# Kernel optimization log

Hardware: AMD Instinct MI355X
Metric: run time of the kernel (lower is better)

Reference implementation:

```python
import jax, jax.numpy as jnp
import numpy as np

N = 100_000   # nodes
E = 3_200_000 # edges
F = 13        # input features
H = 64        # hidden dim
G = 512       # graphs in batch
C = 2         # output classes
BN_EPS = 1e-5


def _linear(key, fan_in, fan_out):
    kw, kb = jax.random.split(key)
    bound = 1.0 / np.sqrt(fan_in)
    W = jax.random.uniform(kw, (fan_in, fan_out), jnp.float32, -bound, bound)
    b = jax.random.uniform(kb, (fan_out,), jnp.float32, -bound, bound)
    return W, b


def _conv_params(key, fin, fout):
    k1, k2, k3 = jax.random.split(key, 3)
    W1, b1 = _linear(k1, fin, fout)
    W2, b2 = _linear(k2, fout, fout)
    gamma = jnp.ones((fout,), jnp.float32)
    beta = jnp.zeros((fout,), jnp.float32)
    mean = jax.random.normal(k3, (fout,), jnp.float32) * 0.1
    var = jnp.ones((fout,), jnp.float32)
    return W1, b1, gamma, beta, mean, var, W2, b2


def setup_inputs() -> dict:
    key = jax.random.key(0)
    ks = jax.random.split(key, 10)
    x = jax.random.normal(ks[0], (N, F), jnp.float32)
    src = jax.random.randint(ks[1], (E,), 0, N, jnp.int32)
    dst = jax.random.randint(ks[2], (E,), 0, N, jnp.int32)
    batch = jnp.sort(jax.random.randint(ks[3], (N,), 0, G, jnp.int32))
    inp = {"x": x, "src": src, "dst": dst, "batch": batch}
    for i, name in enumerate(["c1", "c2", "c3"]):
        fin = F if i == 0 else H
        W1, b1, g, be, m, v, W2, b2 = _conv_params(ks[4 + i], fin, H)
        inp.update({f"{name}_W1": W1, f"{name}_b1": b1, f"{name}_g": g,
                    f"{name}_be": be, f"{name}_m": m, f"{name}_v": v,
                    f"{name}_W2": W2, f"{name}_b2": b2})
    inp["fc1_W"], inp["fc1_b"] = _linear(ks[7], 3 * H, 3 * H)
    inp["fc2_W"], inp["fc2_b"] = _linear(ks[8], 3 * H, C)
    return inp


def _mlp(h, W1, b1, g, be, m, v, W2, b2):
    # Linear -> BatchNorm1d (inference, running stats) -> ReLU -> Linear -> ReLU
    h = h @ W1 + b1
    h = (h - m) * jax.lax.rsqrt(v + BN_EPS) * g + be
    h = jax.nn.relu(h)
    return jax.nn.relu(h @ W2 + b2)


def _gin_conv(x, src, dst, mlp_params):
    # GINConv with eps=0: MLP(x + sum_{j->i} x_j) via scatter-add over edges
    agg = jax.ops.segment_sum(x[src], dst, num_segments=N)
    return _mlp(x + agg, *mlp_params)


def reference(x, src, dst, batch,
              c1_W1, c1_b1, c1_g, c1_be, c1_m, c1_v, c1_W2, c1_b2,
              c2_W1, c2_b1, c2_g, c2_be, c2_m, c2_v, c2_W2, c2_b2,
              c3_W1, c3_b1, c3_g, c3_be, c3_m, c3_v, c3_W2, c3_b2,
              fc1_W, fc1_b, fc2_W, fc2_b):
    h1 = jax.nn.relu(_gin_conv(x, src, dst, (c1_W1, c1_b1, c1_g, c1_be, c1_m, c1_v, c1_W2, c1_b2)))
    h2 = jax.nn.relu(_gin_conv(h1, src, dst, (c2_W1, c2_b1, c2_g, c2_be, c2_m, c2_v, c2_W2, c2_b2)))
    h3 = jax.nn.relu(_gin_conv(h2, src, dst, (c3_W1, c3_b1, c3_g, c3_be, c3_m, c3_v, c3_W2, c3_b2)))
    p1 = jax.ops.segment_sum(h1, batch, num_segments=G)
    p2 = jax.ops.segment_sum(h2, batch, num_segments=G)
    p3 = jax.ops.segment_sum(h3, batch, num_segments=G)
    h = jnp.concatenate([p1, p2, p3], axis=1)  # [G, 3H]
    h = jax.nn.relu(h @ fc1_W + fc1_b)
    # Dropout is identity in eval mode
    h = h @ fc2_W + fc2_b
    return jax.nn.log_softmax(h, axis=-1)
```

## Files before the change

### kernel.cpp

```cpp
#include <hip/hip_runtime.h>

#define NNODES 100000
#define NEDGES 3200000
#define NF 13
#define NFP 16
#define NG 512
#define BN_EPS 1e-5f
#define NTILES (NNODES / 16)

#define BSH 9
#define NBUCK ((NNODES + 511) / 512)
#define PTILE 4096
#define NPBLK ((NEDGES + PTILE - 1) / PTILE)
#define EPT (PTILE / 256)
#define SCAP 17664

#define NCHUNK ((NNODES + 63) / 64)
#define NPTASK (3 * NCHUNK)

typedef __attribute__((ext_vector_type(8))) _Float16 f16x8;
typedef __attribute__((ext_vector_type(4))) _Float16 f16x4;
typedef __attribute__((ext_vector_type(4))) float f32x4;
typedef __attribute__((ext_vector_type(4))) int i32x4;

__device__ __forceinline__ unsigned short f2h(float f) {
    union { _Float16 h; unsigned short u; } c;
    c.h = (_Float16)f;
    return c.u;
}
__device__ __forceinline__ float h2f(unsigned short u) {
    union { _Float16 h; unsigned short u; } c;
    c.u = u;
    return (float)c.h;
}

__device__ __forceinline__ f16x8 shfl_xor8(f16x8 v, int m) {
    union { f16x8 h; int i[4]; } a, b;
    a.h = v;
#pragma unroll
    for (int k = 0; k < 4; ++k) b.i[k] = __shfl_xor(a.i[k], m, 64);
    return b.h;
}
__device__ __forceinline__ f16x4 shfl_xor4(f16x4 v, int m) {
    union { f16x4 h; int i[2]; } a, b;
    a.h = v;
#pragma unroll
    for (int k = 0; k < 2; ++k) b.i[k] = __shfl_xor(a.i[k], m, 64);
    return b.h;
}

__launch_bounds__(256)
__global__ void block_sort_kernel(const int* __restrict__ src, const int* __restrict__ dst,
                                  int* __restrict__ pairout, int* __restrict__ bseg,
                                  int* __restrict__ gcount) {
    __shared__ int hist[256];
    __shared__ int scanbuf[256];
    __shared__ int spair[PTILE];
    int t = threadIdx.x;
    int bid = blockIdx.x;
    int base = bid * PTILE;
    int cnt = NEDGES - base; if (cnt > PTILE) cnt = PTILE;

    int v[EPT], b[EPT];
#pragma unroll
    for (int j = 0; j < EPT; ++j) {
        int i = t + j * 256;
        if (i < cnt) {
            int d = __builtin_nontemporal_load(dst + base + i);
            int s = __builtin_nontemporal_load(src + base + i);
            b[j] = d >> BSH;
            v[j] = ((d & 511) << 17) | s;
        } else b[j] = -1;
    }
    hist[t] = 0;
    __syncthreads();
#pragma unroll
    for (int j = 0; j < EPT; ++j)
        if (b[j] >= 0) atomicAdd(&hist[b[j]], 1);
    __syncthreads();
    int val = hist[t];
    scanbuf[t] = val;
    __syncthreads();
    for (int off = 1; off < 256; off <<= 1) {
        int add = (t >= off) ? scanbuf[t - off] : 0;
        __syncthreads();
        scanbuf[t] += add;
        __syncthreads();
    }
    int excl = scanbuf[t] - val;
    if (t < NBUCK) {
        bseg[(size_t)bid * NBUCK + t] = (excl << 13) | val;
        if (val > 0) atomicAdd(&gcount[t], val);
    }
    hist[t] = excl;
    __syncthreads();
#pragma unroll
    for (int j = 0; j < EPT; ++j) {
        if (b[j] >= 0) {
            int pos = atomicAdd(&hist[b[j]], 1);
            spair[pos] = v[j];
        }
    }
    __syncthreads();
    const i32x4* sp4 = (const i32x4*)spair;
    i32x4* po4 = (i32x4*)(pairout + (size_t)bid * PTILE);
    for (int j = t; j < PTILE / 4; j += 256)
        __builtin_nontemporal_store(sp4[j], po4 + j);
}

__launch_bounds__(1024)
__global__ void bucket_sort_kernel(const int* __restrict__ pairout,
                                   const int* __restrict__ bseg,
                                   const int* __restrict__ gcount,
                                   int* __restrict__ rowptr,
                                   int* __restrict__ csre) {
    __shared__ int scanbuf[1024];
    __shared__ int soff[NPBLK];
    __shared__ int hcur[512];
    __shared__ int shv[2];
    __shared__ int spair[SCAP];
    __shared__ int ssort[SCAP];
    int bk = blockIdx.x;
    int t = threadIdx.x;
    int lo = bk << BSH;
    int wave = t >> 6, lane = t & 63;

    int gv = (t < NBUCK) ? gcount[t] : 0;
    scanbuf[t] = gv;
    __syncthreads();
    for (int off = 1; off < 1024; off <<= 1) {
        int a = (t >= off) ? scanbuf[t - off] : 0;
        __syncthreads();
        scanbuf[t] += a;
        __syncthreads();
    }
    if (t == bk) shv[0] = scanbuf[t] - gv;
    __syncthreads();

    int c = (t < NPBLK) ? (bseg[(size_t)t * NBUCK + bk] & 8191) : 0;
    scanbuf[t] = c;
    __syncthreads();
    for (int off = 1; off < 1024; off <<= 1) {
        int a = (t >= off) ? scanbuf[t - off] : 0;
        __syncthreads();
        scanbuf[t] += a;
        __syncthreads();
    }
    if (t < NPBLK) soff[t] = scanbuf[t] - c;
    if (t == NPBLK - 1) shv[1] = scanbuf[t];
    __syncthreads();
    int bbase = shv[0];
    int total = shv[1]; if (total > SCAP) total = SCAP;

    for (int k = wave; k < NPBLK; k += 16) {
        int pk = bseg[(size_t)k * NBUCK + bk];
        int cnt = pk & 8191;
        const int* seg = pairout + (size_t)k * PTILE + (pk >> 13);
        int dsto = soff[k];
        for (int i = lane; i < cnt; i += 64)
            if (dsto + i < SCAP) spair[dsto + i] = __builtin_nontemporal_load(seg + i);
    }
    if (t < 512) hcur[t] = 0;
    __syncthreads();

    for (int i = t; i < total; i += 1024) atomicAdd(&hcur[spair[i] >> 17], 1);
    __syncthreads();

    int hv = (t < 512) ? hcur[t] : 0;
    scanbuf[t] = hv;
    __syncthreads();
    for (int off = 1; off < 1024; off <<= 1) {
        int a = (t >= off) ? scanbuf[t - off] : 0;
        __syncthreads();
        scanbuf[t] += a;
        __syncthreads();
    }
    if (t < 512) {
        int excl = scanbuf[t] - hv;
        hcur[t] = excl;
        if (lo + t <= NNODES) rowptr[lo + t] = bbase + excl;
    }
    __syncthreads();

    for (int i = t; i < total; i += 1024) {
        int p = spair[i];
        int pos = atomicAdd(&hcur[p >> 17], 1);
        ssort[pos] = p & 0x1FFFF;
    }
    __syncthreads();

    for (int i = t; i < total; i += 1024)
        __builtin_nontemporal_store(ssort[i], csre + bbase + i);
}

#define CVTB 200
__launch_bounds__(256)
__global__ void prep_kernel(const float* __restrict__ x, unsigned short* __restrict__ xh,
                            const float* __restrict__ w10, const float* __restrict__ w20,
                            const float* __restrict__ w11, const float* __restrict__ w21,
                            const float* __restrict__ w12, const float* __restrict__ w22,
                            unsigned short* __restrict__ wfrag) {
    int bid = blockIdx.x;
    int t = threadIdx.x;
    if (bid < 12) {
        int tid = bid * 256 + t;
        if (tid >= 3072) return;
        int layer = tid >> 10;
        int rem = tid & 1023;
        int mat = rem >> 9;
        int tile = (rem >> 7) & 3;
        int chunk = (rem >> 6) & 1;
        int lane = rem & 63;
        int quad = lane >> 4, n = lane & 15;
        const float* W = (layer == 0) ? (mat ? w20 : w10)
                       : (layer == 1) ? (mat ? w21 : w11)
                                      : (mat ? w22 : w12);
        int K = (layer == 0 && mat == 0) ? NF : 64;
        unsigned short* o = wfrag + ((size_t)tid) * 8;
#pragma unroll
        for (int j = 0; j < 8; ++j) {
            int k = chunk * 32 + quad * 8 + j;
            float val = (k < K) ? W[k * 64 + tile * 16 + n] : 0.f;
            o[j] = f2h(val);
        }
    } else {
        const int total = NNODES * NFP;
        int idx = (bid - 12) * 256 + t;
        int stride = CVTB * 256;
        for (int i = idx; i < total; i += stride) {
            int n = i >> 4;
            int f = i & 15;
            xh[i] = (f < NF) ? f2h(__builtin_nontemporal_load(x + n * NF + f))
                             : (unsigned short)0;
        }
    }
}

template <int LAYER>
__launch_bounds__(256, 4)
__global__ void gin_layer_kernel(const unsigned short* __restrict__ xin,
                                 const int* __restrict__ rowptr,
                                 const int* __restrict__ csr,
                                 const unsigned short* __restrict__ wfrag,
                                 const float* __restrict__ b1, const float* __restrict__ gam,
                                 const float* __restrict__ be, const float* __restrict__ mu,
                                 const float* __restrict__ var, const float* __restrict__ b2,
                                 unsigned short* __restrict__ hout) {
    constexpr int FSTR = (LAYER == 1) ? NFP : 64;
    __shared__ __align__(16) unsigned short ytile[16][80];
    __shared__ __align__(16) unsigned short ztile[16][80];
    int lane = threadIdx.x & 63;
    int wid = threadIdx.x >> 6;
    int quad = lane >> 4, n16 = lane & 15;
    int nb = blockIdx.x * 16;

    if constexpr (LAYER == 1) {
        int g = lane >> 2;
        int r = lane & 3;
#pragma unroll
        for (int pp = 0; pp < 2; ++pp) {
            int lnA = wid * 4 + pp * 2;
            int nA = nb + lnA, nB = nA + 1;
            int jA = rowptr[nA];
            int jB = rowptr[nA + 1];
            int endA = jB;
            int endB = rowptr[nA + 2];
            f16x4 accA = {0, 0, 0, 0};
            f16x4 accB = {0, 0, 0, 0};
            if (g == 0) {
                accA = *(const f16x4*)&xin[(size_t)nA * FSTR + r * 4];
                accB = *(const f16x4*)&xin[(size_t)nB * FSTR + r * 4];
            }
            while (jA + 16 <= endA && jB + 16 <= endB) {
                int iA = __builtin_nontemporal_load(csr + jA + g);
                int iB = __builtin_nontemporal_load(csr + jB + g);
                f16x4 vA = *(const f16x4*)&xin[(size_t)iA * FSTR + r * 4];
                f16x4 vB = *(const f16x4*)&xin[(size_t)iB * FSTR + r * 4];
                accA += vA; accB += vB;
                jA += 16; jB += 16;
            }
            for (; jA + 32 <= endA; jA += 32) {
                int i0 = __builtin_nontemporal_load(csr + jA + g);
                int i1 = __builtin_nontemporal_load(csr + jA + 16 + g);
                f16x4 v0 = *(const f16x4*)&xin[(size_t)i0 * FSTR + r * 4];
                f16x4 v1 = *(const f16x4*)&xin[(size_t)i1 * FSTR + r * 4];
                accA += v0; accA += v1;
            }
            for (; jA < endA; jA += 16) {
                int e = jA + g;
                if (e < endA) {
                    int i0 = __builtin_nontemporal_load(csr + e);
                    accA += *(const f16x4*)&xin[(size_t)i0 * FSTR + r * 4];
                }
            }
            for (; jB + 32 <= endB; jB += 32) {
                int i0 = __builtin_nontemporal_load(csr + jB + g);
                int i1 = __builtin_nontemporal_load(csr + jB + 16 + g);
                f16x4 v0 = *(const f16x4*)&xin[(size_t)i0 * FSTR + r * 4];
                f16x4 v1 = *(const f16x4*)&xin[(size_t)i1 * FSTR + r * 4];
                accB += v0; accB += v1;
            }
            for (; jB < endB; jB += 16) {
                int e = jB + g;
                if (e < endB) {
                    int i0 = __builtin_nontemporal_load(csr + e);
                    accB += *(const f16x4*)&xin[(size_t)i0 * FSTR + r * 4];
                }
            }
#pragma unroll
            for (int m = 4; m < 64; m <<= 1) {
                accA += shfl_xor4(accA, m);
                accB += shfl_xor4(accB, m);
            }
            if (g == 0) {
                *(f16x4*)&ytile[lnA][r * 4] = accA;
                *(f16x4*)&ytile[lnA + 1][r * 4] = accB;
            } else if (g == 1) {
                f16x4 z = {0, 0, 0, 0};
                *(f16x4*)&ytile[lnA][16 + r * 4] = z;
                *(f16x4*)&ytile[lnA + 1][16 + r * 4] = z;
            }
        }
    } else {
        int g = lane >> 3;
        int r = lane & 7;
#pragma unroll
        for (int pp = 0; pp < 2; ++pp) {
            int lnA = wid * 4 + pp * 2;
            int nA = nb + lnA, nB = nA + 1;
            int jA = rowptr[nA];
            int jB = rowptr[nA + 1];
            int endA = jB;
            int endB = rowptr[nA + 2];
            f16x8 accA = {0, 0, 0, 0, 0, 0, 0, 0};
            f16x8 accB = {0, 0, 0, 0, 0, 0, 0, 0};
            if (g == 0) {
                accA = *(const f16x8*)&xin[(size_t)nA * 64 + r * 8];
                accB = *(const f16x8*)&xin[(size_t)nB * 64 + r * 8];
            }
            while (jA + 16 <= endA && jB + 16 <= endB) {
                int iA0 = __builtin_nontemporal_load(csr + jA + g);
                int iA1 = __builtin_nontemporal_load(csr + jA + 8 + g);
                int iB0 = __builtin_nontemporal_load(csr + jB + g);
                int iB1 = __builtin_nontemporal_load(csr + jB + 8 + g);
                f16x8 vA0 = *(const f16x8*)&xin[(size_t)iA0 * 64 + r * 8];
                f16x8 vA1 = *(const f16x8*)&xin[(size_t)iA1 * 64 + r * 8];
                f16x8 vB0 = *(const f16x8*)&xin[(size_t)iB0 * 64 + r * 8];
                f16x8 vB1 = *(const f16x8*)&xin[(size_t)iB1 * 64 + r * 8];
                accA += vA0; accA += vA1;
                accB += vB0; accB += vB1;
                jA += 16; jB += 16;
            }
            for (; jA + 16 <= endA; jA += 16) {
                int i0 = __builtin_nontemporal_load(csr + jA + g);
                int i1 = __builtin_nontemporal_load(csr + jA + 8 + g);
                f16x8 v0 = *(const f16x8*)&xin[(size_t)i0 * 64 + r * 8];
                f16x8 v1 = *(const f16x8*)&xin[(size_t)i1 * 64 + r * 8];
                accA += v0; accA += v1;
            }
            for (; jA < endA; jA += 8) {
                int e = jA + g;
                if (e < endA) {
                    int i0 = __builtin_nontemporal_load(csr + e);
                    accA += *(const f16x8*)&xin[(size_t)i0 * 64 + r * 8];
                }
            }
            for (; jB + 16 <= endB; jB += 16) {
                int i0 = __builtin_nontemporal_load(csr + jB + g);
                int i1 = __builtin_nontemporal_load(csr + jB + 8 + g);
                f16x8 v0 = *(const f16x8*)&xin[(size_t)i0 * 64 + r * 8];
                f16x8 v1 = *(const f16x8*)&xin[(size_t)i1 * 64 + r * 8];
                accB += v0; accB += v1;
            }
            for (; jB < endB; jB += 8) {
                int e = jB + g;
                if (e < endB) {
                    int i0 = __builtin_nontemporal_load(csr + e);
                    accB += *(const f16x8*)&xin[(size_t)i0 * 64 + r * 8];
                }
            }
#pragma unroll
            for (int m = 8; m < 64; m <<= 1) {
                accA += shfl_xor8(accA, m);
                accB += shfl_xor8(accB, m);
            }
            if (g == 0) {
                *(f16x8*)&ytile[lnA][r * 8] = accA;
                *(f16x8*)&ytile[lnA + 1][r * 8] = accB;
            }
        }
    }

    const f16x8* wf = (const f16x8*)wfrag;
    f16x8 w1f0 = wf[((0 * 4 + wid) * 2 + 0) * 64 + lane];
    f16x8 w1f1 = (LAYER == 2) ? wf[((0 * 4 + wid) * 2 + 1) * 64 + lane] : w1f0;
    f16x8 w2f0 = wf[((1 * 4 + wid) * 2 + 0) * 64 + lane];
    f16x8 w2f1 = wf[((1 * 4 + wid) * 2 + 1) * 64 + lane];
    int f = wid * 16 + n16;
    float sc = gam[f] * rsqrtf(var[f] + BN_EPS);
    float sh = (b1[f] - mu[f]) * sc + be[f];
    float bb2 = b2[f];

    __syncthreads();

    f16x8 a0 = *(const f16x8*)&ytile[n16][quad * 8];
    f32x4 z4 = {0.f, 0.f, 0.f, 0.f};
    z4 = __builtin_amdgcn_mfma_f32_16x16x32_f16(a0, w1f0, z4, 0, 0, 0);
    if constexpr (LAYER == 2) {
        f16x8 a1 = *(const f16x8*)&ytile[n16][32 + quad * 8];
        z4 = __builtin_amdgcn_mfma_f32_16x16x32_f16(a1, w1f1, z4, 0, 0, 0);
    }
#pragma unroll
    for (int reg = 0; reg < 4; ++reg) {
        float z = fmaxf(fmaf(z4[reg], sc, sh), 0.f);
        ztile[quad * 4 + reg][wid * 16 + n16] = f2h(z);
    }
    __syncthreads();

    f16x8 az0 = *(const f16x8*)&ztile[n16][quad * 8];
    f16x8 az1 = *(const f16x8*)&ztile[n16][32 + quad * 8];
    f32x4 h4 = {0.f, 0.f, 0.f, 0.f};
    h4 = __builtin_amdgcn_mfma_f32_16x16x32_f16(az0, w2f0, h4, 0, 0, 0);
    h4 = __builtin_amdgcn_mfma_f32_16x16x32_f16(az1, w2f1, h4, 0, 0, 0);
#pragma unroll
    for (int reg = 0; reg < 4; ++reg) {
        float h = fmaxf(h4[reg] + bb2, 0.f);
        hout[(size_t)(nb + quad * 4 + reg) * 64 + wid * 16 + n16] = f2h(h);
    }
}

__launch_bounds__(256)
__global__ void pool_kernel(const unsigned short* __restrict__ h1,
                            const unsigned short* __restrict__ h2,
                            const unsigned short* __restrict__ h3,
                            const int* __restrict__ batch,
                            float* __restrict__ pool) {
    int task = blockIdx.x * 4 + (threadIdx.x >> 6);
    if (task >= NPTASK) return;
    int lane = threadIdx.x & 63;
    int layer = task / NCHUNK;
    int c = task - layer * NCHUNK;
    int n0 = c * 64;
    int n1 = n0 + 64; if (n1 > NNODES) n1 = NNODES;
    const unsigned short* hb = (layer == 0) ? h1 : (layer == 1) ? h2 : h3;
    float acc = 0.f;
    int curg = batch[n0];
    for (int n = n0; n < n1; ++n) {
        int gid = batch[n];
        if (gid != curg) {
            atomicAdd(&pool[(size_t)curg * 192 + layer * 64 + lane], acc);
            acc = 0.f;
            curg = gid;
        }
        acc += h2f(__builtin_nontemporal_load(hb + (size_t)n * 64 + lane));
    }
    atomicAdd(&pool[(size_t)curg * 192 + layer * 64 + lane], acc);
}

__global__ void head_kernel(const float* __restrict__ pool,
                            const float* __restrict__ fc1W, const float* __restrict__ fc1b,
                            const float* __restrict__ fc2W, const float* __restrict__ fc2b,
                            float* __restrict__ out) {
    __shared__ float ps[192];
    __shared__ float hs[192];
    int gi = blockIdx.x;
    int t = threadIdx.x;
    ps[t] = pool[gi * 192 + t];
    __syncthreads();
    float acc = fc1b[t];
#pragma unroll 8
    for (int k = 0; k < 192; ++k) acc = fmaf(ps[k], fc1W[k * 192 + t], acc);
    hs[t] = fmaxf(acc, 0.f);
    __syncthreads();
    if (t == 0) {
        float l0 = fc2b[0], l1 = fc2b[1];
        for (int k = 0; k < 192; ++k) {
            float h = hs[k];
            l0 = fmaf(h, fc2W[k * 2 + 0], l0);
            l1 = fmaf(h, fc2W[k * 2 + 1], l1);
        }
        float mx = fmaxf(l0, l1);
        float lse = mx + logf(expf(l0 - mx) + expf(l1 - mx));
        out[gi * 2 + 0] = l0 - lse;
        out[gi * 2 + 1] = l1 - lse;
    }
}

extern "C" void kernel_launch(void* const* d_in, const int* in_sizes, int n_in,
                              void* d_out, int out_size, void* d_ws, size_t ws_size,
                              hipStream_t stream) {
    const float* x = (const float*)d_in[0];
    const int* src = (const int*)d_in[1];
    const int* dst = (const int*)d_in[2];
    const int* batch = (const int*)d_in[3];
    const float* c1[8];
    const float* c2[8];
    const float* c3[8];
    for (int i = 0; i < 8; ++i) {
        c1[i] = (const float*)d_in[4 + i];
        c2[i] = (const float*)d_in[12 + i];
        c3[i] = (const float*)d_in[20 + i];
    }
    const float* fc1W = (const float*)d_in[28];
    const float* fc1b = (const float*)d_in[29];
    const float* fc2W = (const float*)d_in[30];
    const float* fc2b = (const float*)d_in[31];
    float* out = (float*)d_out;

    unsigned short* base = (unsigned short*)d_ws;
    const size_t NA = (size_t)NNODES * 64;
    unsigned short* xh  = base;
    unsigned short* h1  = xh + (size_t)NNODES * NFP;
    unsigned short* h2  = h1 + NA;
    unsigned short* h3  = h2 + NA;
    unsigned short* wfrag = h3 + NA;
    float* pool = (float*)(wfrag + 3 * 8192);
    int* ibase = (int*)(pool + (size_t)NG * 192);
    int* rowptr  = ibase;
    int* gcount  = rowptr + NNODES + 1;
    int* csre    = gcount + NBUCK + 63;
    int* pairout = csre + NEDGES + 256;
    int* bseg    = pairout + (size_t)NPBLK * PTILE;

    (void)hipMemsetAsync(gcount, 0, NBUCK * sizeof(int), stream);
    (void)hipMemsetAsync(pool, 0, (size_t)NG * 192 * sizeof(float), stream);

    block_sort_kernel<<<NPBLK, 256, 0, stream>>>(src, dst, pairout, bseg, gcount);
    prep_kernel<<<12 + CVTB, 256, 0, stream>>>(
        x, xh, c1[0], c1[6], c2[0], c2[6], c3[0], c3[6], wfrag);
    bucket_sort_kernel<<<NBUCK, 1024, 0, stream>>>(pairout, bseg, gcount, rowptr, csre);

    gin_layer_kernel<1><<<NTILES, 256, 0, stream>>>(
        xh, rowptr, csre, wfrag + 0 * 8192,
        c1[1], c1[2], c1[3], c1[4], c1[5], c1[7], h1);
    gin_layer_kernel<2><<<NTILES, 256, 0, stream>>>(
        h1, rowptr, csre, wfrag + 1 * 8192,
        c2[1], c2[2], c2[3], c2[4], c2[5], c2[7], h2);
    gin_layer_kernel<2><<<NTILES, 256, 0, stream>>>(
        h2, rowptr, csre, wfrag + 2 * 8192,
        c3[1], c3[2], c3[3], c3[4], c3[5], c3[7], h3);

    pool_kernel<<<(NPTASK + 3) / 4, 256, 0, stream>>>(h1, h2, h3, batch, pool);
    head_kernel<<<NG, 192, 0, stream>>>(pool, fc1W, fc1b, fc2W, fc2b, out);
}
```

Before: 446.4 us.

## Fuse prep into sort, use fixed-capacity CSR buckets, merge pooling into head

Merges the block sort and prep/weight-fragment conversion into one launch. The global bucket-count prefix is dropped by giving each bucket a fixed SCAP-sized slot in the CSR array, with per-node (start,end) pairs replacing rowptr. Pooling and the head MLP become one kernel per graph, which binary-searches the sorted batch array for its node range and sums it without atomics, so the two memsets go away. This saves launches, atomics and a scan. In exchange the CSR array is larger and padded, and per-graph pooling runs as serial loops over ~200 nodes per block.

```diff
diff --git a/kernel.cpp b/kernel.cpp
--- a/kernel.cpp
+++ b/kernel.cpp
@@ -14,9 +14,8 @@
 #define NPBLK ((NEDGES + PTILE - 1) / PTILE)
 #define EPT (PTILE / 256)
 #define SCAP 17664
-
-#define NCHUNK ((NNODES + 63) / 64)
-#define NPTASK (3 * NCHUNK)
+#define CVTB 200
+#define K1B (NPBLK + 12 + CVTB)
 
 typedef __attribute__((ext_vector_type(8))) _Float16 f16x8;
 typedef __attribute__((ext_vector_type(4))) _Float16 f16x4;
@@ -50,160 +49,66 @@
 }
 
 __launch_bounds__(256)
-__global__ void block_sort_kernel(const int* __restrict__ src, const int* __restrict__ dst,
-                                  int* __restrict__ pairout, int* __restrict__ bseg,
-                                  int* __restrict__ gcount) {
+__global__ void prep_sort_kernel(const int* __restrict__ src, const int* __restrict__ dst,
+                                 int* __restrict__ pairout, int* __restrict__ bseg,
+                                 const float* __restrict__ x, unsigned short* __restrict__ xh,
+                                 const float* __restrict__ w10, const float* __restrict__ w20,
+                                 const float* __restrict__ w11, const float* __restrict__ w21,
+                                 const float* __restrict__ w12, const float* __restrict__ w22,
+                                 unsigned short* __restrict__ wfrag) {
     __shared__ int hist[256];
     __shared__ int scanbuf[256];
     __shared__ int spair[PTILE];
     int t = threadIdx.x;
     int bid = blockIdx.x;
-    int base = bid * PTILE;
-    int cnt = NEDGES - base; if (cnt > PTILE) cnt = PTILE;
-
-    int v[EPT], b[EPT];
-#pragma unroll
-    for (int j = 0; j < EPT; ++j) {
-        int i = t + j * 256;
-        if (i < cnt) {
-            int d = __builtin_nontemporal_load(dst + base + i);
-            int s = __builtin_nontemporal_load(src + base + i);
-            b[j] = d >> BSH;
-            v[j] = ((d & 511) << 17) | s;
-        } else b[j] = -1;
-    }
-    hist[t] = 0;
-    __syncthreads();
-#pragma unroll
-    for (int j = 0; j < EPT; ++j)
-        if (b[j] >= 0) atomicAdd(&hist[b[j]], 1);
-    __syncthreads();
-    int val = hist[t];
-    scanbuf[t] = val;
-    __syncthreads();
-    for (int off = 1; off < 256; off <<= 1) {
-        int add = (t >= off) ? scanbuf[t - off] : 0;
-        __syncthreads();
-        scanbuf[t] += add;
-        __syncthreads();
-    }
-    int excl = scanbuf[t] - val;
-    if (t < NBUCK) {
-        bseg[(size_t)bid * NBUCK + t] = (excl << 13) | val;
-        if (val > 0) atomicAdd(&gcount[t], val);
-    }
-    hist[t] = excl;
-    __syncthreads();
-#pragma unroll
-    for (int j = 0; j < EPT; ++j) {
-        if (b[j] >= 0) {
-            int pos = atomicAdd(&hist[b[j]], 1);
-            spair[pos] = v[j];
-        }
-    }
-    __syncthreads();
-    const i32x4* sp4 = (const i32x4*)spair;
-    i32x4* po4 = (i32x4*)(pairout + (size_t)bid * PTILE);
-    for (int j = t; j < PTILE / 4; j += 256)
-        __builtin_nontemporal_store(sp4[j], po4 + j);
-}
-
-__launch_bounds__(1024)
-__global__ void bucket_sort_kernel(const int* __restrict__ pairout,
-                                   const int* __restrict__ bseg,
-                                   const int* __restrict__ gcount,
-                                   int* __restrict__ rowptr,
-                                   int* __restrict__ csre) {
-    __shared__ int scanbuf[1024];
-    __shared__ int soff[NPBLK];
-    __shared__ int hcur[512];
-    __shared__ int shv[2];
-    __shared__ int spair[SCAP];
-    __shared__ int ssort[SCAP];
-    int bk = blockIdx.x;
-    int t = threadIdx.x;
-    int lo = bk << BSH;
-    int wave = t >> 6, lane = t & 63;
-
-    int gv = (t < NBUCK) ? gcount[t] : 0;
-    scanbuf[t] = gv;
-    __syncthreads();
-    for (int off = 1; off < 1024; off <<= 1) {
-        int a = (t >= off) ? scanbuf[t - off] : 0;
-        __syncthreads();
-        scanbuf[t] += a;
-        __syncthreads();
-    }
-    if (t == bk) shv[0] = scanbuf[t] - gv;
-    __syncthreads();
-
-    int c = (t < NPBLK) ? (bseg[(size_t)t * NBUCK + bk] & 8191) : 0;
-    scanbuf[t] = c;
-    __syncthreads();
-    for (int off = 1; off < 1024; off <<= 1) {
-        int a = (t >= off) ? scanbuf[t - off] : 0;
-        __syncthreads();
-        scanbuf[t] += a;
-        __syncthreads();
-    }
-    if (t < NPBLK) soff[t] = scanbuf[t] - c;
-    if (t == NPBLK - 1) shv[1] = scanbuf[t];
-    __syncthreads();
-    int bbase = shv[0];
-    int total = shv[1]; if (total > SCAP) total = SCAP;
-
-    for (int k = wave; k < NPBLK; k += 16) {
-        int pk = bseg[(size_t)k * NBUCK + bk];
-        int cnt = pk & 8191;
-        const int* seg = pairout + (size_t)k * PTILE + (pk >> 13);
-        int dsto = soff[k];
-        for (int i = lane; i < cnt; i += 64)
-            if (dsto + i < SCAP) spair[dsto + i] = __builtin_nontemporal_load(seg + i);
-    }
-    if (t < 512) hcur[t] = 0;
-    __syncthreads();
-
-    for (int i = t; i < total; i += 1024) atomicAdd(&hcur[spair[i] >> 17], 1);
-    __syncthreads();
-
-    int hv = (t < 512) ? hcur[t] : 0;
-    scanbuf[t] = hv;
-    __syncthreads();
-    for (int off = 1; off < 1024; off <<= 1) {
-        int a = (t >= off) ? scanbuf[t - off] : 0;
-        __syncthreads();
-        scanbuf[t] += a;
-        __syncthreads();
-    }
-    if (t < 512) {
-        int excl = scanbuf[t] - hv;
-        hcur[t] = excl;
-        if (lo + t <= NNODES) rowptr[lo + t] = bbase + excl;
-    }
-    __syncthreads();
-
-    for (int i = t; i < total; i += 1024) {
-        int p = spair[i];
-        int pos = atomicAdd(&hcur[p >> 17], 1);
-        ssort[pos] = p & 0x1FFFF;
-    }
-    __syncthreads();
-
-    for (int i = t; i < total; i += 1024)
-        __builtin_nontemporal_store(ssort[i], csre + bbase + i);
-}
-
-#define CVTB 200
-__launch_bounds__(256)
-__global__ void prep_kernel(const float* __restrict__ x, unsigned short* __restrict__ xh,
-                            const float* __restrict__ w10, const float* __restrict__ w20,
-                            const float* __restrict__ w11, const float* __restrict__ w21,
-                            const float* __restrict__ w12, const float* __restrict__ w22,
-                            unsigned short* __restrict__ wfrag) {
-    int bid = blockIdx.x;
-    int t = threadIdx.x;
-    if (bid < 12) {
-        int tid = bid * 256 + t;
+
+    if (bid < NPBLK) {
+        int base = bid * PTILE;
+        int cnt = NEDGES - base; if (cnt > PTILE) cnt = PTILE;
+        int v[EPT], b[EPT];
+#pragma unroll
+        for (int j = 0; j < EPT; ++j) {
+            int i = t + j * 256;
+            if (i < cnt) {
+                int d = __builtin_nontemporal_load(dst + base + i);
+                int s = __builtin_nontemporal_load(src + base + i);
+                b[j] = d >> BSH;
+                v[j] = ((d & 511) << 17) | s;
+            } else b[j] = -1;
+        }
+        hist[t] = 0;
+        __syncthreads();
+#pragma unroll
+        for (int j = 0; j < EPT; ++j)
+            if (b[j] >= 0) atomicAdd(&hist[b[j]], 1);
+        __syncthreads();
+        int val = hist[t];
+        scanbuf[t] = val;
+        __syncthreads();
+        for (int off = 1; off < 256; off <<= 1) {
+            int add = (t >= off) ? scanbuf[t - off] : 0;
+            __syncthreads();
+            scanbuf[t] += add;
+            __syncthreads();
+        }
+        int excl = scanbuf[t] - val;
+        if (t < NBUCK) bseg[(size_t)bid * NBUCK + t] = (excl << 13) | val;
+        hist[t] = excl;
+        __syncthreads();
+#pragma unroll
+        for (int j = 0; j < EPT; ++j) {
+            if (b[j] >= 0) {
+                int pos = atomicAdd(&hist[b[j]], 1);
+                spair[pos] = v[j];
+            }
+        }
+        __syncthreads();
+        const i32x4* sp4 = (const i32x4*)spair;
+        i32x4* po4 = (i32x4*)(pairout + (size_t)bid * PTILE);
+        for (int j = t; j < PTILE / 4; j += 256)
+            __builtin_nontemporal_store(sp4[j], po4 + j);
+    } else if (bid < NPBLK + 12) {
+        int tid = (bid - NPBLK) * 256 + t;
         if (tid >= 3072) return;
         int layer = tid >> 10;
         int rem = tid & 1023;
@@ -225,7 +130,7 @@
         }
     } else {
         const int total = NNODES * NFP;
-        int idx = (bid - 12) * 256 + t;
+        int idx = (bid - NPBLK - 12) * 256 + t;
         int stride = CVTB * 256;
         for (int i = idx; i < total; i += stride) {
             int n = i >> 4;
@@ -236,10 +141,85 @@
     }
 }
 
+__launch_bounds__(1024)
+__global__ void bucket_sort_kernel(const int* __restrict__ pairout,
+                                   const int* __restrict__ bseg,
+                                   int2* __restrict__ rowse,
+                                   int* __restrict__ csre) {
+    __shared__ int scanbuf[1024];
+    __shared__ int soff[NPBLK];
+    __shared__ int hcur[512];
+    __shared__ int shv[1];
+    __shared__ int spair[SCAP];
+    __shared__ int ssort[SCAP];
+    int bk = blockIdx.x;
+    int t = threadIdx.x;
+    int lo = bk << BSH;
+    int wave = t >> 6, lane = t & 63;
+    int bbase = bk * SCAP;
+
+    int c = (t < NPBLK) ? (bseg[(size_t)t * NBUCK + bk] & 8191) : 0;
+    scanbuf[t] = c;
+    __syncthreads();
+    for (int off = 1; off < 1024; off <<= 1) {
+        int a = (t >= off) ? scanbuf[t - off] : 0;
+        __syncthreads();
+        scanbuf[t] += a;
+        __syncthreads();
+    }
+    if (t < NPBLK) soff[t] = scanbuf[t] - c;
+    if (t == NPBLK - 1) shv[0] = scanbuf[t];
+    __syncthreads();
+    int total = shv[0]; if (total > SCAP) total = SCAP;
+
+    for (int k = wave; k < NPBLK; k += 16) {
+        int pk = bseg[(size_t)k * NBUCK + bk];
+        int cnt = pk & 8191;
+        const int* seg = pairout + (size_t)k * PTILE + (pk >> 13);
+        int dsto = soff[k];
+        for (int i = lane; i < cnt; i += 64)
+            if (dsto + i < SCAP) spair[dsto + i] = __builtin_nontemporal_load(seg + i);
+    }
+    if (t < 512) hcur[t] = 0;
+    __syncthreads();
+
+    for (int i = t; i < total; i += 1024) atomicAdd(&hcur[spair[i] >> 17], 1);
+    __syncthreads();
+
+    int hv = (t < 512) ? hcur[t] : 0;
+    scanbuf[t] = hv;
+    __syncthreads();
+    for (int off = 1; off < 1024; off <<= 1) {
+        int a = (t >= off) ? scanbuf[t - off] : 0;
+        __syncthreads();
+        scanbuf[t] += a;
+        __syncthreads();
+    }
+    if (t < 512) {
+        int excl = scanbuf[t] - hv;
+        hcur[t] = excl;
+        if (lo + t < NNODES) {
+            int2 se; se.x = bbase + excl; se.y = bbase + excl + hv;
+            rowse[lo + t] = se;
+        }
+    }
+    __syncthreads();
+
+    for (int i = t; i < total; i += 1024) {
+        int p = spair[i];
+        int pos = atomicAdd(&hcur[p >> 17], 1);
+        ssort[pos] = p & 0x1FFFF;
+    }
+    __syncthreads();
+
+    for (int i = t; i < total; i += 1024)
+        __builtin_nontemporal_store(ssort[i], csre + bbase + i);
+}
+
 template <int LAYER>
 __launch_bounds__(256, 4)
 __global__ void gin_layer_kernel(const unsigned short* __restrict__ xin,
-                                 const int* __restrict__ rowptr,
+                                 const int2* __restrict__ rowse,
                                  const int* __restrict__ csr,
                                  const unsigned short* __restrict__ wfrag,
                                  const float* __restrict__ b1, const float* __restrict__ gam,
@@ -261,10 +241,10 @@
         for (int pp = 0; pp < 2; ++pp) {
             int lnA = wid * 4 + pp * 2;
             int nA = nb + lnA, nB = nA + 1;
-            int jA = rowptr[nA];
-            int jB = rowptr[nA + 1];
-            int endA = jB;
-            int endB = rowptr[nA + 2];
+            int2 seA = rowse[nA];
+            int2 seB = rowse[nB];
+            int jA = seA.x, endA = seA.y;
+            int jB = seB.x, endB = seB.y;
             f16x4 accA = {0, 0, 0, 0};
             f16x4 accB = {0, 0, 0, 0};
             if (g == 0) {
@@ -328,10 +308,10 @@
         for (int pp = 0; pp < 2; ++pp) {
             int lnA = wid * 4 + pp * 2;
             int nA = nb + lnA, nB = nA + 1;
-            int jA = rowptr[nA];
-            int jB = rowptr[nA + 1];
-            int endA = jB;
-            int endB = rowptr[nA + 2];
+            int2 seA = rowse[nA];
+            int2 seB = rowse[nB];
+            int jA = seA.x, endA = seA.y;
+            int jB = seB.x, endB = seB.y;
             f16x8 accA = {0, 0, 0, 0, 0, 0, 0, 0};
             f16x8 accB = {0, 0, 0, 0, 0, 0, 0, 0};
             if (g == 0) {
@@ -429,48 +409,38 @@
     }
 }
 
-__launch_bounds__(256)
-__global__ void pool_kernel(const unsigned short* __restrict__ h1,
-                            const unsigned short* __restrict__ h2,
-                            const unsigned short* __restrict__ h3,
-                            const int* __restrict__ batch,
-                            float* __restrict__ pool) {
-    int task = blockIdx.x * 4 + (threadIdx.x >> 6);
-    if (task >= NPTASK) return;
-    int lane = threadIdx.x & 63;
-    int layer = task / NCHUNK;
-    int c = task - layer * NCHUNK;
-    int n0 = c * 64;
-    int n1 = n0 + 64; if (n1 > NNODES) n1 = NNODES;
-    const unsigned short* hb = (layer == 0) ? h1 : (layer == 1) ? h2 : h3;
-    float acc = 0.f;
-    int curg = batch[n0];
-    for (int n = n0; n < n1; ++n) {
-        int gid = batch[n];
-        if (gid != curg) {
-            atomicAdd(&pool[(size_t)curg * 192 + layer * 64 + lane], acc);
-            acc = 0.f;
-            curg = gid;
-        }
-        acc += h2f(__builtin_nontemporal_load(hb + (size_t)n * 64 + lane));
-    }
-    atomicAdd(&pool[(size_t)curg * 192 + layer * 64 + lane], acc);
-}
-
-__global__ void head_kernel(const float* __restrict__ pool,
-                            const float* __restrict__ fc1W, const float* __restrict__ fc1b,
-                            const float* __restrict__ fc2W, const float* __restrict__ fc2b,
-                            float* __restrict__ out) {
+__launch_bounds__(192)
+__global__ void poolhead_kernel(const unsigned short* __restrict__ h1,
+                                const unsigned short* __restrict__ h2,
+                                const unsigned short* __restrict__ h3,
+                                const int* __restrict__ batch,
+                                const float* __restrict__ fc1W, const float* __restrict__ fc1b,
+                                const float* __restrict__ fc2W, const float* __restrict__ fc2b,
+                                float* __restrict__ out) {
     __shared__ float ps[192];
     __shared__ float hs[192];
     int gi = blockIdx.x;
     int t = threadIdx.x;
-    ps[t] = pool[gi * 192 + t];
-    __syncthreads();
-    float acc = fc1b[t];
+
+    int l = 0, r = NNODES;
+    while (l < r) { int m = (l + r) >> 1; if (batch[m] < gi) l = m + 1; else r = m; }
+    int lo = l;
+    r = NNODES;
+    while (l < r) { int m = (l + r) >> 1; if (batch[m] < gi + 1) l = m + 1; else r = m; }
+    int hi = l;
+
+    int layer = t >> 6, lane = t & 63;
+    const unsigned short* hb = (layer == 0) ? h1 : (layer == 1) ? h2 : h3;
+    float acc = 0.f;
+    for (int n = lo; n < hi; ++n)
+        acc += h2f(__builtin_nontemporal_load(hb + (size_t)n * 64 + lane));
+    ps[t] = acc;
+    __syncthreads();
+
+    float a = fc1b[t];
 #pragma unroll 8
-    for (int k = 0; k < 192; ++k) acc = fmaf(ps[k], fc1W[k * 192 + t], acc);
-    hs[t] = fmaxf(acc, 0.f);
+    for (int k = 0; k < 192; ++k) a = fmaf(ps[k], fc1W[k * 192 + t], a);
+    hs[t] = fmaxf(a, 0.f);
     __syncthreads();
     if (t == 0) {
         float l0 = fc2b[0], l1 = fc2b[1];
@@ -514,32 +484,28 @@
     unsigned short* h2  = h1 + NA;
     unsigned short* h3  = h2 + NA;
     unsigned short* wfrag = h3 + NA;
-    float* pool = (float*)(wfrag + 3 * 8192);
-    int* ibase = (int*)(pool + (size_t)NG * 192);
-    int* rowptr  = ibase;
-    int* gcount  = rowptr + NNODES + 1;
-    int* csre    = gcount + NBUCK + 63;
-    int* pairout = csre + NEDGES + 256;
+    int* ibase = (int*)(wfrag + 3 * 8192);
+    int2* rowse  = (int2*)ibase;
+    int* csre    = ibase + 2 * NNODES;
+    int* pairout = csre + (size_t)NBUCK * SCAP + 256;
     int* bseg    = pairout + (size_t)NPBLK * PTILE;
 
-    (void)hipMemsetAsync(gcount, 0, NBUCK * sizeof(int), stream);
-    (void)hipMemsetAsync(pool, 0, (size_t)NG * 192 * sizeof(float), stream);
-
-    block_sort_kernel<<<NPBLK, 256, 0, stream>>>(src, dst, pairout, bseg, gcount);
-    prep_kernel<<<12 + CVTB, 256, 0, stream>>>(
-        x, xh, c1[0], c1[6], c2[0], c2[6], c3[0], c3[6], wfrag);
-    bucket_sort_kernel<<<NBUCK, 1024, 0, stream>>>(pairout, bseg, gcount, rowptr, csre);
+    prep_sort_kernel<<<K1B, 256, 0, stream>>>(
+        src, dst, pairout, bseg, x, xh,
+        c1[0], c1[6], c2[0], c2[6], c3[0], c3[6], wfrag);
+
+    bucket_sort_kernel<<<NBUCK, 1024, 0, stream>>>(pairout, bseg, rowse, csre);
 
     gin_layer_kernel<1><<<NTILES, 256, 0, stream>>>(
-        xh, rowptr, csre, wfrag + 0 * 8192,
+        xh, rowse, csre, wfrag + 0 * 8192,
         c1[1], c1[2], c1[3], c1[4], c1[5], c1[7], h1);
     gin_layer_kernel<2><<<NTILES, 256, 0, stream>>>(
-        h1, rowptr, csre, wfrag + 1 * 8192,
+        h1, rowse, csre, wfrag + 1 * 8192,
         c2[1], c2[2], c2[3], c2[4], c2[5], c2[7], h2);
     gin_layer_kernel<2><<<NTILES, 256, 0, stream>>>(
-        h2, rowptr, csre, wfrag + 2 * 8192,
+        h2, rowse, csre, wfrag + 2 * 8192,
         c3[1], c3[2], c3[3], c3[4], c3[5], c3[7], h3);
 
-    pool_kernel<<<(NPTASK + 3) / 4, 256, 0, stream>>>(h1, h2, h3, batch, pool);
-    head_kernel<<<NG, 192, 0, stream>>>(pool, fc1W, fc1b, fc2W, fc2b, out);
-}
+    poolhead_kernel<<<NG, 192, 0, stream>>>(
+        h1, h2, h3, batch, fc1W, fc1b, fc2W, fc2b, out);
+}
```

After: 443.9 us. About the same (-0.6%).
